# Optimization experiments

Hardware: AMD Instinct MI355X
Metric: run time of the kernel (lower is better)

The kernel has to match this reference:

```python
import jax, jax.numpy as jnp
import numpy as np

M = 10000; D = 10000; FG = 256; FD = 256; K = 64
EX = 320000; EY = 320000


def setup_inputs() -> dict:
    key = jax.random.key(0)
    ks = jax.random.split(key, 32)
    s = 0.05  # weight scale
    inp = {}
    inp['x_m'] = jax.random.normal(ks[0], (M, FG), jnp.float32)
    inp['x_d'] = jax.random.normal(ks[1], (D, FD), jnp.float32)
    inp['edge_index_x'] = jax.random.randint(ks[2], (2, EX), 0, M)
    inp['edge_index_y'] = jax.random.randint(ks[3], (2, EY), 0, D)
    # GAT layer params (PyG layout: W [in, H*C], att [H, C], bias [H*C])
    inp['Wx1'] = jax.random.normal(ks[4], (FG, 2 * FG), jnp.float32) * s
    inp['ax1_src'] = jax.random.normal(ks[5], (2, FG), jnp.float32) * s
    inp['ax1_dst'] = jax.random.normal(ks[6], (2, FG), jnp.float32) * s
    inp['bx1'] = jnp.zeros((2 * FG,), jnp.float32)
    inp['Wx2'] = jax.random.normal(ks[7], (2 * FG, FG), jnp.float32) * s
    inp['ax2_src'] = jax.random.normal(ks[8], (1, FG), jnp.float32) * s
    inp['ax2_dst'] = jax.random.normal(ks[9], (1, FG), jnp.float32) * s
    inp['bx2'] = jnp.zeros((FG,), jnp.float32)
    inp['Wy1'] = jax.random.normal(ks[10], (FD, 2 * FD), jnp.float32) * s
    inp['ay1_src'] = jax.random.normal(ks[11], (2, FD), jnp.float32) * s
    inp['ay1_dst'] = jax.random.normal(ks[12], (2, FD), jnp.float32) * s
    inp['by1'] = jnp.zeros((2 * FD,), jnp.float32)
    inp['Wy2'] = jax.random.normal(ks[13], (2 * FD, FD), jnp.float32) * s
    inp['ay2_src'] = jax.random.normal(ks[14], (1, FD), jnp.float32) * s
    inp['ay2_dst'] = jax.random.normal(ks[15], (1, FD), jnp.float32) * s
    inp['by2'] = jnp.zeros((FD,), jnp.float32)
    # MLP heads
    inp['lwx1'] = jax.random.normal(ks[16], (FG, 256), jnp.float32) * s
    inp['lbx1'] = jnp.zeros((256,), jnp.float32)
    inp['lwx2'] = jax.random.normal(ks[17], (256, 128), jnp.float32) * s
    inp['lbx2'] = jnp.zeros((128,), jnp.float32)
    inp['lwx3'] = jax.random.normal(ks[18], (128, K), jnp.float32) * s
    inp['lbx3'] = jnp.zeros((K,), jnp.float32)
    inp['lwy1'] = jax.random.normal(ks[19], (FD, 256), jnp.float32) * s
    inp['lby1'] = jnp.zeros((256,), jnp.float32)
    inp['lwy2'] = jax.random.normal(ks[20], (256, 128), jnp.float32) * s
    inp['lby2'] = jnp.zeros((128,), jnp.float32)
    inp['lwy3'] = jax.random.normal(ks[21], (128, K), jnp.float32) * s
    inp['lby3'] = jnp.zeros((K,), jnp.float32)
    return inp


def gat_conv(x, src, dst, W, a_src, a_dst, b, n):
    # PyG GATConv, add_self_loops=False, negative_slope=0.2, concat=True
    H, C = a_src.shape
    xp = (x @ W).reshape(-1, H, C)                      # [N, H, C]
    al_s = jnp.einsum('nhc,hc->nh', xp, a_src)          # [N, H]
    al_d = jnp.einsum('nhc,hc->nh', xp, a_dst)
    e = jax.nn.leaky_relu(al_s[src] + al_d[dst], 0.2)   # [E, H]
    # softmax over edges grouped by destination node
    mx = jax.ops.segment_max(e, dst, num_segments=n)
    ee = jnp.exp(e - mx[dst])
    denom = jax.ops.segment_sum(ee, dst, num_segments=n)
    alpha = ee / (denom[dst] + 1e-16)                   # [E, H]
    out = jax.ops.segment_sum(xp[src] * alpha[:, :, None], dst, num_segments=n)
    return out.reshape(n, H * C) + b


def mlp3(h, w1, b1, w2, b2, w3, b3):
    h = jax.nn.relu(h @ w1 + b1)
    h = jax.nn.relu(h @ w2 + b2)
    return jax.nn.relu(h @ w3 + b3)


def reference(x_m, x_d, edge_index_x, edge_index_y,
              Wx1, ax1_src, ax1_dst, bx1, Wx2, ax2_src, ax2_dst, bx2,
              Wy1, ay1_src, ay1_dst, by1, Wy2, ay2_src, ay2_dst, by2,
              lwx1, lbx1, lwx2, lbx2, lwx3, lbx3,
              lwy1, lby1, lwy2, lby2, lwy3, lby3):
    sx, dx = edge_index_x[0], edge_index_x[1]
    sy, dy = edge_index_y[0], edge_index_y[1]
    X1 = jax.nn.relu(gat_conv(x_m, sx, dx, Wx1, ax1_src, ax1_dst, bx1, M))
    X = jax.nn.relu(gat_conv(X1, sx, dx, Wx2, ax2_src, ax2_dst, bx2, M))
    Y1 = jax.nn.relu(gat_conv(x_d, sy, dy, Wy1, ay1_src, ay1_dst, by1, D))
    Y = jax.nn.relu(gat_conv(Y1, sy, dy, Wy2, ay2_src, ay2_dst, by2, D))
    x = mlp3(X, lwx1, lbx1, lwx2, lbx2, lwx3, lbx3)     # [M, K]
    y = mlp3(Y, lwy1, lby1, lwy2, lby2, lwy3, lby3)     # [D, K]
    return x @ y.T                                      # [M, D]
```

## Files before the change

kernel.cpp:

```cpp
#include <hip/hip_runtime.h>
#include <cstddef>

#define NODES 10000
#define EDGES 320000

typedef __attribute__((ext_vector_type(8))) short bf16x8;
typedef __attribute__((ext_vector_type(4))) float f32x4;

__device__ inline short bf16rn(float x){
    union { float f; unsigned u; } v; v.f = x;
    unsigned r = (v.u + 0x7FFFu + ((v.u >> 16) & 1u)) >> 16;
    return (short)r;
}
__device__ inline float bf16tof(short h){
    union { float f; unsigned u; } v; v.u = ((unsigned)(unsigned short)h) << 16;
    return v.f;
}

__global__ void count_kernel(const int* __restrict__ dst, int E, int* __restrict__ counts){
    int e = blockIdx.x*blockDim.x + threadIdx.x;
    if (e < E) atomicAdd(&counts[dst[e]], 1);
}

__global__ __launch_bounds__(1024) void scan_kernel(const int* __restrict__ counts,
                                                    int* __restrict__ rowptr, int N){
    __shared__ int part[1024];
    int t = threadIdx.x;
    int chunk = (N + 1023) / 1024;
    int b0 = t * chunk;
    int s = 0;
    for (int i=0;i<chunk;i++){ int idx=b0+i; if (idx<N) s += counts[idx]; }
    part[t] = s;
    __syncthreads();
    for (int off=1; off<1024; off<<=1){
        int v = (t>=off) ? part[t-off] : 0;
        __syncthreads();
        part[t] += v;
        __syncthreads();
    }
    int excl = (t==0) ? 0 : part[t-1];
    for (int i=0;i<chunk;i++){
        int idx=b0+i;
        if (idx<N){ rowptr[idx]=excl; excl += counts[idx]; }
    }
    if (t==1023) rowptr[N] = part[1023];
}

__global__ void fill_kernel(const int* __restrict__ src, const int* __restrict__ dst, int E,
                            int* __restrict__ cursor, int* __restrict__ col){
    int e = blockIdx.x*blockDim.x + threadIdx.x;
    if (e < E){
        int d = dst[e];
        int p = atomicAdd(&cursor[d], 1);
        col[p] = src[e];
    }
}

__global__ __launch_bounds__(256) void splitT(const float* __restrict__ B,
        short* __restrict__ Bth, short* __restrict__ Btl, int K, int N)
{
    __shared__ float tile[32][33];
    int tx = threadIdx.x, ty = threadIdx.y;
    int n0 = blockIdx.x * 32, k0 = blockIdx.y * 32;
    #pragma unroll
    for (int r=0;r<4;r++){
        int k = ty + r*8;
        tile[k][tx] = B[(size_t)(k0+k)*N + n0 + tx];
    }
    __syncthreads();
    #pragma unroll
    for (int r=0;r<4;r++){
        int n = ty + r*8;
        float v = tile[tx][n];
        short h = bf16rn(v);
        short l = bf16rn(v - bf16tof(h));
        Bth[(size_t)(n0+n)*K + k0 + tx] = h;
        Btl[(size_t)(n0+n)*K + k0 + tx] = l;
    }
}

__global__ void split_rows(const float* __restrict__ in, short* __restrict__ hi,
                           short* __restrict__ lo, int n)
{
    int i = (blockIdx.x*blockDim.x + threadIdx.x) * 4;
    if (i >= n) return;
    float4 v = *(const float4*)&in[i];
    short h0=bf16rn(v.x), h1=bf16rn(v.y), h2=bf16rn(v.z), h3=bf16rn(v.w);
    short4 hv; hv.x=h0; hv.y=h1; hv.z=h2; hv.w=h3;
    short4 lv; lv.x=bf16rn(v.x-bf16tof(h0)); lv.y=bf16rn(v.y-bf16tof(h1));
    lv.z=bf16rn(v.z-bf16tof(h2)); lv.w=bf16rn(v.w-bf16tof(h3));
    *(short4*)&hi[i] = hv;
    *(short4*)&lo[i] = lv;
}

__global__ __launch_bounds__(256) void gemm_split(
    const float* __restrict__ A,
    const short* __restrict__ Bh, const short* __restrict__ Bl,
    float* __restrict__ C, const float* __restrict__ bias,
    int Mr, int Nr, int Kr, int relu)
{
    constexpr int LD = 88;
    __shared__ short Ash[64][LD], Asl[64][LD], Bsh[64][LD], Bsl[64][LD];
    int t = threadIdx.x;
    int lane = t & 63, wave = t >> 6;
    int wm = (wave >> 1) * 32, wn = (wave & 1) * 32;
    int m0 = blockIdx.y * 64, n0 = blockIdx.x * 64;

    f32x4 acc[2][2];
    #pragma unroll
    for (int i=0;i<2;i++)
      #pragma unroll
      for (int j=0;j<2;j++)
        #pragma unroll
        for (int r=0;r<4;r++) acc[i][j][r] = 0.f;

    int ar = t >> 4;
    int ac = (t & 15) * 4;
    int br = t >> 3;
    int bc = (t & 7) * 8;

    for (int k0 = 0; k0 < Kr; k0 += 64){
        #pragma unroll
        for (int rep = 0; rep < 4; rep++){
            int row = ar + rep*16;
            float4 v = make_float4(0.f,0.f,0.f,0.f);
            if (m0 + row < Mr) v = *(const float4*)&A[(size_t)(m0+row)*Kr + k0 + ac];
            short h0=bf16rn(v.x), h1=bf16rn(v.y), h2=bf16rn(v.z), h3=bf16rn(v.w);
            short4 hv; hv.x=h0; hv.y=h1; hv.z=h2; hv.w=h3;
            short4 lv; lv.x=bf16rn(v.x-bf16tof(h0)); lv.y=bf16rn(v.y-bf16tof(h1));
            lv.z=bf16rn(v.z-bf16tof(h2)); lv.w=bf16rn(v.w-bf16tof(h3));
            *(short4*)&Ash[row][ac] = hv;
            *(short4*)&Asl[row][ac] = lv;
        }
        #pragma unroll
        for (int rep = 0; rep < 2; rep++){
            int row = br + rep*32;
            int gn = n0 + row;
            int4 hv = make_int4(0,0,0,0), lv = make_int4(0,0,0,0);
            if (gn < Nr){
                hv = *(const int4*)&Bh[(size_t)gn*Kr + k0 + bc];
                lv = *(const int4*)&Bl[(size_t)gn*Kr + k0 + bc];
            }
            *(int4*)&Bsh[row][bc] = hv;
            *(int4*)&Bsl[row][bc] = lv;
        }
        __syncthreads();
        #pragma unroll
        for (int ks = 0; ks < 2; ks++){
            int kk = ks*32 + (lane >> 4) * 8;
            bf16x8 ah[2], alo[2], bh[2], blo[2];
            #pragma unroll
            for (int i=0;i<2;i++){
                ah[i]  = *(const bf16x8*)&Ash[wm + i*16 + (lane&15)][kk];
                alo[i] = *(const bf16x8*)&Asl[wm + i*16 + (lane&15)][kk];
                bh[i]  = *(const bf16x8*)&Bsh[wn + i*16 + (lane&15)][kk];
                blo[i] = *(const bf16x8*)&Bsl[wn + i*16 + (lane&15)][kk];
            }
            #pragma unroll
            for (int i=0;i<2;i++)
              #pragma unroll
              for (int j=0;j<2;j++){
                  acc[i][j] = __builtin_amdgcn_mfma_f32_16x16x32_bf16(ah[i],  bh[j],  acc[i][j], 0,0,0);
                  acc[i][j] = __builtin_amdgcn_mfma_f32_16x16x32_bf16(alo[i], bh[j],  acc[i][j], 0,0,0);
                  acc[i][j] = __builtin_amdgcn_mfma_f32_16x16x32_bf16(ah[i],  blo[j], acc[i][j], 0,0,0);
              }
        }
        __syncthreads();
    }
    #pragma unroll
    for (int i=0;i<2;i++){
        int rbase = m0 + wm + i*16 + (lane>>4)*4;
        #pragma unroll
        for (int j=0;j<2;j++){
            int col = n0 + wn + j*16 + (lane&15);
            if (col >= Nr) continue;
            float bv = bias ? bias[col] : 0.f;
            #pragma unroll
            for (int r=0;r<4;r++){
                int row = rbase + r;
                if (row < Mr){
                    float v = acc[i][j][r] + bv;
                    if (relu) v = v > 0.f ? v : 0.f;
                    C[(size_t)row*Nr + col] = v;
                }
            }
        }
    }
}

__global__ __launch_bounds__(256) void al_kernel(const float* __restrict__ xp,
        const float* __restrict__ a_src, const float* __restrict__ a_dst,
        float* __restrict__ als, float* __restrict__ ald, int N, int H, int C)
{
    int n = blockIdx.x;
    int t = threadIdx.x;
    __shared__ float rs[4], rd[4];
    for (int h=0;h<H;h++){
        float ps=0.f, pd=0.f;
        for (int c=t;c<C;c+=256){
            float v = xp[(size_t)n*H*C + (size_t)h*C + c];
            ps += v * a_src[h*C+c];
            pd += v * a_dst[h*C+c];
        }
        #pragma unroll
        for (int off=32; off; off>>=1){
            ps += __shfl_down(ps, off);
            pd += __shfl_down(pd, off);
        }
        if ((t & 63) == 0){ rs[t>>6]=ps; rd[t>>6]=pd; }
        __syncthreads();
        if (t==0){
            als[n*H+h] = rs[0]+rs[1]+rs[2]+rs[3];
            ald[n*H+h] = rd[0]+rd[1]+rd[2]+rd[3];
        }
        __syncthreads();
    }
}

template<int H, int C>
__global__ __launch_bounds__(256) void gat_agg(const float* __restrict__ xp,
        const float* __restrict__ als, const float* __restrict__ ald,
        const int* __restrict__ rowptr, const int* __restrict__ col,
        const float* __restrict__ bias, float* __restrict__ out, int N)
{
    constexpr int W  = H*C;
    constexpr int PC = W/256;
    constexpr int CH = 128;
    int n = blockIdx.x;
    int t = threadIdx.x;
    int beg = rowptr[n], end = rowptr[n+1];
    int deg = end - beg;
    __shared__ float red[4];
    __shared__ float m_sh[H], den_sh[H];
    __shared__ int   sidx[CH];
    __shared__ float salpha[CH*H];

    float aldn[H];
    #pragma unroll
    for (int h=0;h<H;h++) aldn[h] = ald[n*H+h];

    for (int h=0;h<H;h++){
        float mx = -1e30f;
        for (int i=t;i<deg;i+=256){
            int s = col[beg+i];
            float e = als[s*H+h] + aldn[h];
            e = e>0.f ? e : 0.2f*e;
            mx = fmaxf(mx, e);
        }
        #pragma unroll
        for (int off=32; off; off>>=1) mx = fmaxf(mx, __shfl_down(mx,off));
        if ((t&63)==0) red[t>>6]=mx;
        __syncthreads();
        if (t==0) m_sh[h] = fmaxf(fmaxf(red[0],red[1]), fmaxf(red[2],red[3]));
        __syncthreads();
        float m = m_sh[h];
        float sm = 0.f;
        for (int i=t;i<deg;i+=256){
            int s = col[beg+i];
            float e = als[s*H+h] + aldn[h];
            e = e>0.f ? e : 0.2f*e;
            sm += expf(e - m);
        }
        #pragma unroll
        for (int off=32; off; off>>=1) sm += __shfl_down(sm,off);
        if ((t&63)==0) red[t>>6]=sm;
        __syncthreads();
        if (t==0) den_sh[h] = red[0]+red[1]+red[2]+red[3];
        __syncthreads();
    }

    float acc[PC];
    #pragma unroll
    for (int j=0;j<PC;j++) acc[j]=0.f;
    float invden[H], msh[H];
    #pragma unroll
    for (int h=0;h<H;h++){ invden[h] = 1.f/(den_sh[h]+1e-16f); msh[h]=m_sh[h]; }

    for (int c0=0;c0<deg;c0+=CH){
        int cl = min(CH, deg-c0);
        __syncthreads();
        if (t < cl){
            int s = col[beg+c0+t];
            sidx[t] = s;
            #pragma unroll
            for (int h=0;h<H;h++){
                float e = als[s*H+h] + aldn[h];
                e = e>0.f ? e : 0.2f*e;
                salpha[t*H+h] = expf(e - msh[h]) * invden[h];
            }
        }
        __syncthreads();
        for (int i=0;i<cl;i++){
            int s = sidx[i];
            const float* row = xp + (size_t)s*W;
            #pragma unroll
            for (int j=0;j<PC;j++){
                int cidx = t + j*256;
                acc[j] += salpha[i*H + (cidx/C)] * row[cidx];
            }
        }
    }
    #pragma unroll
    for (int j=0;j<PC;j++){
        int cidx = t + j*256;
        float v = acc[j] + bias[cidx];
        out[(size_t)n*W + cidx] = v>0.f ? v : 0.f;
    }
}

extern "C" void kernel_launch(void* const* d_in, const int* in_sizes, int n_in,
                              void* d_out, int out_size, void* d_ws, size_t ws_size,
                              hipStream_t stream)
{
    const float* x_m  = (const float*)d_in[0];
    const float* x_d  = (const float*)d_in[1];
    const int*   eix  = (const int*)d_in[2];
    const int*   eiy  = (const int*)d_in[3];
    const float* Wx1  = (const float*)d_in[4];
    const float* ax1s = (const float*)d_in[5];
    const float* ax1d = (const float*)d_in[6];
    const float* bx1  = (const float*)d_in[7];
    const float* Wx2  = (const float*)d_in[8];
    const float* ax2s = (const float*)d_in[9];
    const float* ax2d = (const float*)d_in[10];
    const float* bx2  = (const float*)d_in[11];
    const float* Wy1  = (const float*)d_in[12];
    const float* ay1s = (const float*)d_in[13];
    const float* ay1d = (const float*)d_in[14];
    const float* by1  = (const float*)d_in[15];
    const float* Wy2  = (const float*)d_in[16];
    const float* ay2s = (const float*)d_in[17];
    const float* ay2d = (const float*)d_in[18];
    const float* by2  = (const float*)d_in[19];
    const float* lwx1 = (const float*)d_in[20];
    const float* lbx1 = (const float*)d_in[21];
    const float* lwx2 = (const float*)d_in[22];
    const float* lbx2 = (const float*)d_in[23];
    const float* lwx3 = (const float*)d_in[24];
    const float* lbx3 = (const float*)d_in[25];
    const float* lwy1 = (const float*)d_in[26];
    const float* lby1 = (const float*)d_in[27];
    const float* lwy2 = (const float*)d_in[28];
    const float* lby2 = (const float*)d_in[29];
    const float* lwy3 = (const float*)d_in[30];
    const float* lby3 = (const float*)d_in[31];

    const int N = NODES, E = EDGES;
    char* ws = (char*)d_ws;
    size_t off = 0;
    auto alloc = [&](size_t bytes)->char*{
        size_t a = (off + 255) & ~(size_t)255;
        off = a + bytes;
        return ws + a;
    };
    int* rowptr   = (int*)alloc((size_t)(N+1)*sizeof(int));
    int* cursor   = (int*)alloc((size_t)N*sizeof(int));
    int* counts   = (int*)alloc((size_t)N*sizeof(int));
    int* colidx   = (int*)alloc((size_t)E*sizeof(int));
    float* xp     = (float*)alloc((size_t)N*512*sizeof(float));
    float* bufA   = (float*)alloc((size_t)N*512*sizeof(float));
    float* bufB   = (float*)alloc((size_t)N*256*sizeof(float));
    float* als    = (float*)alloc((size_t)N*2*sizeof(float));
    float* aldv   = (float*)alloc((size_t)N*2*sizeof(float));
    float* xf     = (float*)alloc((size_t)N*64*sizeof(float));
    float* yf     = (float*)alloc((size_t)N*64*sizeof(float));
    short* Bth    = (short*)alloc((size_t)512*512*sizeof(short));
    short* Btl    = (short*)alloc((size_t)512*512*sizeof(short));
    short* Yh     = (short*)alloc((size_t)N*64*sizeof(short));
    short* Yl     = (short*)alloc((size_t)N*64*sizeof(short));

    auto gemm = [&](const float* A, const float* W, float* C, const float* bias,
                    int Kr, int Nr, int relu)
    {
        splitT<<<dim3(Nr/32, Kr/32), dim3(32,8), 0, stream>>>(W, Bth, Btl, Kr, Nr);
        gemm_split<<<dim3((Nr+63)/64, (N+63)/64), 256, 0, stream>>>(
            A, Bth, Btl, C, bias, N, Nr, Kr, relu);
    };

    auto run_graph = [&](const float* xin, const int* ei,
                         const float* W1, const float* a1s, const float* a1d, const float* b1,
                         const float* W2, const float* a2s, const float* a2d, const float* b2,
                         const float* lw1, const float* lb1, const float* lw2, const float* lb2,
                         const float* lw3, const float* lb3, float* outv)
    {
        const int* srcp = ei;
        const int* dstp = ei + E;
        hipMemsetAsync(counts, 0, (size_t)N*sizeof(int), stream);
        count_kernel<<<(E+255)/256, 256, 0, stream>>>(dstp, E, counts);
        scan_kernel<<<1, 1024, 0, stream>>>(counts, rowptr, N);
        hipMemcpyAsync(cursor, rowptr, (size_t)N*sizeof(int), hipMemcpyDeviceToDevice, stream);
        fill_kernel<<<(E+255)/256, 256, 0, stream>>>(srcp, dstp, E, cursor, colidx);
        gemm(xin, W1, xp, nullptr, 256, 512, 0);
        al_kernel<<<N, 256, 0, stream>>>(xp, a1s, a1d, als, aldv, N, 2, 256);
        gat_agg<2,256><<<N, 256, 0, stream>>>(xp, als, aldv, rowptr, colidx, b1, bufA, N);
        gemm(bufA, W2, xp, nullptr, 512, 256, 0);
        al_kernel<<<N, 256, 0, stream>>>(xp, a2s, a2d, als, aldv, N, 1, 256);
        gat_agg<1,256><<<N, 256, 0, stream>>>(xp, als, aldv, rowptr, colidx, b2, bufB, N);
        gemm(bufB, lw1, bufA, lb1, 256, 256, 1);
        gemm(bufA, lw2, xp,   lb2, 256, 128, 1);
        gemm(xp,   lw3, outv, lb3, 128, 64,  1);
    };

    run_graph(x_m, eix, Wx1, ax1s, ax1d, bx1, Wx2, ax2s, ax2d, bx2,
              lwx1, lbx1, lwx2, lbx2, lwx3, lbx3, xf);
    run_graph(x_d, eiy, Wy1, ay1s, ay1d, by1, Wy2, ay2s, ay2d, by2,
              lwy1, lby1, lwy2, lby2, lwy3, lby3, yf);

    split_rows<<<(N*64/4 + 255)/256, 256, 0, stream>>>(yf, Yh, Yl, N*64);
    gemm_split<<<dim3((N+63)/64, (N+63)/64), 256, 0, stream>>>(
        xf, Yh, Yl, (float*)d_out, nullptr, N, N, 64, 0);
}
```

Measured before the change: 1.258 ms.

## Batch both graphs into shared kernels with presplit bf16 operands and precomputed attention

Processes the two graphs together: a combined CSR build, batched weight splitting, and two-job GEMM launches, so each stage runs as one launch instead of two. GEMM outputs are written directly as hi/lo bf16 pairs, which removes the per-tile fp32-to-bf16 split inside the GEMM. Attention logits come from a precomputed W·a vector (a GEMV on the layer input) instead of a pass over the projected features. Softmax coefficients are computed in a separate per-edge kernel before aggregation. The GEMM tile grows to 96 rows. The cost is more workspace memory and extra kernels for alpha and weight preprocessing.

Measured after the change: 1.148 ms. 1.1x faster.

```diff
diff --git a/kernel.cpp b/kernel.cpp
--- a/kernel.cpp
+++ b/kernel.cpp
@@ -1,5 +1,6 @@
 #include <hip/hip_runtime.h>
 #include <cstddef>
+#include <cstdint>
 
 #define NODES 10000
 #define EDGES 320000
@@ -17,9 +18,13 @@
     return v.f;
 }
 
-__global__ void count_kernel(const int* __restrict__ dst, int E, int* __restrict__ counts){
-    int e = blockIdx.x*blockDim.x + threadIdx.x;
-    if (e < E) atomicAdd(&counts[dst[e]], 1);
+__global__ void count2_kernel(const int* __restrict__ ex, const int* __restrict__ ey,
+                              int* __restrict__ counts){
+    int e = blockIdx.x*256 + threadIdx.x;
+    if (e < 2*EDGES){
+        int d = (e < EDGES) ? ex[EDGES + e] : (ey[e] + NODES);
+        atomicAdd(&counts[d], 1);
+    }
 }
 
 __global__ __launch_bounds__(1024) void scan_kernel(const int* __restrict__ counts,
@@ -46,265 +51,278 @@
     if (t==1023) rowptr[N] = part[1023];
 }
 
-__global__ void fill_kernel(const int* __restrict__ src, const int* __restrict__ dst, int E,
-                            int* __restrict__ cursor, int* __restrict__ col){
-    int e = blockIdx.x*blockDim.x + threadIdx.x;
-    if (e < E){
-        int d = dst[e];
+__global__ void fill2_kernel(const int* __restrict__ ex, const int* __restrict__ ey,
+                             int* __restrict__ cursor, int* __restrict__ col){
+    int e = blockIdx.x*256 + threadIdx.x;
+    if (e < 2*EDGES){
+        int s, d;
+        if (e < EDGES){ s = ex[e]; d = ex[EDGES+e]; }
+        else          { s = ey[e-EDGES] + NODES; d = ey[e] + NODES; }
         int p = atomicAdd(&cursor[d], 1);
-        col[p] = src[e];
-    }
-}
-
-__global__ __launch_bounds__(256) void splitT(const float* __restrict__ B,
-        short* __restrict__ Bth, short* __restrict__ Btl, int K, int N)
-{
+        col[p] = s;
+    }
+}
+
+struct WtJob { const float* W; const float* a; float* out; int K; int H; int h; };
+struct WtJobs { WtJob j[12]; };
+__global__ __launch_bounds__(256) void wtilde_kernel(WtJobs js){
+    WtJob jb = js.j[blockIdx.x];
+    const int C = 256;
+    for (int k = threadIdx.x; k < jb.K; k += 256){
+        const float* wr = jb.W + (size_t)k*(jb.H*C) + jb.h*C;
+        const float* ar = jb.a + jb.h*C;
+        float s = 0.f;
+        for (int c=0;c<C;c++) s += wr[c]*ar[c];
+        jb.out[k*jb.H + jb.h] = s;
+    }
+}
+
+struct StJob { const float* B; short* th; short* tl; int K; int N; };
+struct StJobs { StJob j[10]; };
+__global__ __launch_bounds__(256) void splitT_batch(StJobs js){
+    StJob jb = js.j[blockIdx.z];
+    int n0 = blockIdx.x*32, k0 = blockIdx.y*32;
+    if (n0 >= jb.N || k0 >= jb.K) return;
     __shared__ float tile[32][33];
     int tx = threadIdx.x, ty = threadIdx.y;
-    int n0 = blockIdx.x * 32, k0 = blockIdx.y * 32;
-    #pragma unroll
-    for (int r=0;r<4;r++){
-        int k = ty + r*8;
-        tile[k][tx] = B[(size_t)(k0+k)*N + n0 + tx];
-    }
+    #pragma unroll
+    for (int r=0;r<4;r++){ int k = ty + r*8; tile[k][tx] = jb.B[(size_t)(k0+k)*jb.N + n0 + tx]; }
     __syncthreads();
     #pragma unroll
     for (int r=0;r<4;r++){
         int n = ty + r*8;
         float v = tile[tx][n];
         short h = bf16rn(v);
-        short l = bf16rn(v - bf16tof(h));
-        Bth[(size_t)(n0+n)*K + k0 + tx] = h;
-        Btl[(size_t)(n0+n)*K + k0 + tx] = l;
-    }
-}
-
-__global__ void split_rows(const float* __restrict__ in, short* __restrict__ hi,
-                           short* __restrict__ lo, int n)
-{
-    int i = (blockIdx.x*blockDim.x + threadIdx.x) * 4;
-    if (i >= n) return;
-    float4 v = *(const float4*)&in[i];
+        jb.th[(size_t)(n0+n)*jb.K + k0 + tx] = h;
+        jb.tl[(size_t)(n0+n)*jb.K + k0 + tx] = bf16rn(v - bf16tof(h));
+    }
+}
+
+__global__ void split_in_kernel(const float* __restrict__ x0, const float* __restrict__ x1,
+                                short* __restrict__ h, short* __restrict__ l){
+    int i = (blockIdx.x*256 + threadIdx.x)*4;
+    const int HALF = NODES*256;
+    if (i >= 2*HALF) return;
+    const float* src = (i < HALF) ? (x0 + i) : (x1 + (i - HALF));
+    float4 v = *(const float4*)src;
     short h0=bf16rn(v.x), h1=bf16rn(v.y), h2=bf16rn(v.z), h3=bf16rn(v.w);
     short4 hv; hv.x=h0; hv.y=h1; hv.z=h2; hv.w=h3;
     short4 lv; lv.x=bf16rn(v.x-bf16tof(h0)); lv.y=bf16rn(v.y-bf16tof(h1));
     lv.z=bf16rn(v.z-bf16tof(h2)); lv.w=bf16rn(v.w-bf16tof(h3));
-    *(short4*)&hi[i] = hv;
-    *(short4*)&lo[i] = lv;
-}
-
-__global__ __launch_bounds__(256) void gemm_split(
-    const float* __restrict__ A,
-    const short* __restrict__ Bh, const short* __restrict__ Bl,
-    float* __restrict__ C, const float* __restrict__ bias,
-    int Mr, int Nr, int Kr, int relu)
+    *(short4*)&h[i] = hv;
+    *(short4*)&l[i] = lv;
+}
+
+struct GemmJob {
+    const short* Ah; const short* Al; const short* Bh; const short* Bl;
+    float* C; short* Ch; short* Cl; const float* bias;
+};
+__global__ __launch_bounds__(256) void gemm_ps(GemmJob j0, GemmJob j1,
+        int Mr, int Nr, int Kr, int relu)
 {
-    constexpr int LD = 88;
-    __shared__ short Ash[64][LD], Asl[64][LD], Bsh[64][LD], Bsl[64][LD];
+    GemmJob j = (blockIdx.z == 0) ? j0 : j1;
+    __shared__ short Ash[96][88], Asl[96][88], Bsh[64][88], Bsl[64][88];
     int t = threadIdx.x;
     int lane = t & 63, wave = t >> 6;
-    int wm = (wave >> 1) * 32, wn = (wave & 1) * 32;
-    int m0 = blockIdx.y * 64, n0 = blockIdx.x * 64;
-
-    f32x4 acc[2][2];
-    #pragma unroll
-    for (int i=0;i<2;i++)
+    int wm = (wave >> 1) * 48, wn = (wave & 1) * 32;
+    int m0 = blockIdx.y * 96, n0 = blockIdx.x * 64;
+
+    f32x4 acc[3][2];
+    #pragma unroll
+    for (int i=0;i<3;i++)
       #pragma unroll
-      for (int j=0;j<2;j++)
-        #pragma unroll
-        for (int r=0;r<4;r++) acc[i][j][r] = 0.f;
-
-    int ar = t >> 4;
-    int ac = (t & 15) * 4;
-    int br = t >> 3;
-    int bc = (t & 7) * 8;
+      for (int jj=0;jj<2;jj++)
+        #pragma unroll
+        for (int r=0;r<4;r++) acc[i][jj][r] = 0.f;
+
+    int arow = t >> 3;
+    int ablk = (t & 7) * 8;
 
     for (int k0 = 0; k0 < Kr; k0 += 64){
         #pragma unroll
-        for (int rep = 0; rep < 4; rep++){
-            int row = ar + rep*16;
-            float4 v = make_float4(0.f,0.f,0.f,0.f);
-            if (m0 + row < Mr) v = *(const float4*)&A[(size_t)(m0+row)*Kr + k0 + ac];
-            short h0=bf16rn(v.x), h1=bf16rn(v.y), h2=bf16rn(v.z), h3=bf16rn(v.w);
-            short4 hv; hv.x=h0; hv.y=h1; hv.z=h2; hv.w=h3;
-            short4 lv; lv.x=bf16rn(v.x-bf16tof(h0)); lv.y=bf16rn(v.y-bf16tof(h1));
-            lv.z=bf16rn(v.z-bf16tof(h2)); lv.w=bf16rn(v.w-bf16tof(h3));
-            *(short4*)&Ash[row][ac] = hv;
-            *(short4*)&Asl[row][ac] = lv;
-        }
-        #pragma unroll
-        for (int rep = 0; rep < 2; rep++){
-            int row = br + rep*32;
-            int gn = n0 + row;
-            int4 hv = make_int4(0,0,0,0), lv = make_int4(0,0,0,0);
-            if (gn < Nr){
-                hv = *(const int4*)&Bh[(size_t)gn*Kr + k0 + bc];
-                lv = *(const int4*)&Bl[(size_t)gn*Kr + k0 + bc];
-            }
-            *(int4*)&Bsh[row][bc] = hv;
-            *(int4*)&Bsl[row][bc] = lv;
+        for (int rep=0; rep<3; rep++){
+            int row = arow + rep*32;
+            int gr = m0 + row; gr = gr < Mr ? gr : Mr-1;
+            size_t off = (size_t)gr*Kr + k0 + ablk;
+            *(int4*)&Ash[row][ablk] = *(const int4*)&j.Ah[off];
+            *(int4*)&Asl[row][ablk] = *(const int4*)&j.Al[off];
+        }
+        #pragma unroll
+        for (int rep=0; rep<2; rep++){
+            int row = arow + rep*32;
+            int gn = n0 + row; gn = gn < Nr ? gn : Nr-1;
+            size_t off = (size_t)gn*Kr + k0 + ablk;
+            *(int4*)&Bsh[row][ablk] = *(const int4*)&j.Bh[off];
+            *(int4*)&Bsl[row][ablk] = *(const int4*)&j.Bl[off];
         }
         __syncthreads();
         #pragma unroll
-        for (int ks = 0; ks < 2; ks++){
-            int kk = ks*32 + (lane >> 4) * 8;
-            bf16x8 ah[2], alo[2], bh[2], blo[2];
+        for (int ks=0; ks<2; ks++){
+            int kk = ks*32 + (lane>>4)*8;
+            bf16x8 bh[2], bl[2];
             #pragma unroll
-            for (int i=0;i<2;i++){
-                ah[i]  = *(const bf16x8*)&Ash[wm + i*16 + (lane&15)][kk];
-                alo[i] = *(const bf16x8*)&Asl[wm + i*16 + (lane&15)][kk];
-                bh[i]  = *(const bf16x8*)&Bsh[wn + i*16 + (lane&15)][kk];
-                blo[i] = *(const bf16x8*)&Bsl[wn + i*16 + (lane&15)][kk];
+            for (int jj=0;jj<2;jj++){
+                bh[jj] = *(const bf16x8*)&Bsh[wn + jj*16 + (lane&15)][kk];
+                bl[jj] = *(const bf16x8*)&Bsl[wn + jj*16 + (lane&15)][kk];
             }
             #pragma unroll
-            for (int i=0;i<2;i++)
-              #pragma unroll
-              for (int j=0;j<2;j++){
-                  acc[i][j] = __builtin_amdgcn_mfma_f32_16x16x32_bf16(ah[i],  bh[j],  acc[i][j], 0,0,0);
-                  acc[i][j] = __builtin_amdgcn_mfma_f32_16x16x32_bf16(alo[i], bh[j],  acc[i][j], 0,0,0);
-                  acc[i][j] = __builtin_amdgcn_mfma_f32_16x16x32_bf16(ah[i],  blo[j], acc[i][j], 0,0,0);
-              }
+            for (int i=0;i<3;i++){
+                bf16x8 ah = *(const bf16x8*)&Ash[wm + i*16 + (lane&15)][kk];
+                bf16x8 al = *(const bf16x8*)&Asl[wm + i*16 + (lane&15)][kk];
+                #pragma unroll
+                for (int jj=0;jj<2;jj++){
+                    acc[i][jj] = __builtin_amdgcn_mfma_f32_16x16x32_bf16(ah, bh[jj], acc[i][jj], 0,0,0);
+                    acc[i][jj] = __builtin_amdgcn_mfma_f32_16x16x32_bf16(al, bh[jj], acc[i][jj], 0,0,0);
+                    acc[i][jj] = __builtin_amdgcn_mfma_f32_16x16x32_bf16(ah, bl[jj], acc[i][jj], 0,0,0);
+                }
+            }
         }
         __syncthreads();
     }
     #pragma unroll
-    for (int i=0;i<2;i++){
-        int rbase = m0 + wm + i*16 + (lane>>4)*4;
-        #pragma unroll
-        for (int j=0;j<2;j++){
-            int col = n0 + wn + j*16 + (lane&15);
-            if (col >= Nr) continue;
-            float bv = bias ? bias[col] : 0.f;
+    for (int i=0;i<3;i++){
+        int rbase = m0 + wm + i*16 + ((lane>>4)<<2);
+        #pragma unroll
+        for (int jj=0;jj<2;jj++){
+            int colg = n0 + wn + jj*16 + (lane&15);
+            if (colg >= Nr) continue;
+            float bv = j.bias ? j.bias[colg] : 0.f;
             #pragma unroll
             for (int r=0;r<4;r++){
-                int row = rbase + r;
-                if (row < Mr){
-                    float v = acc[i][j][r] + bv;
+                int rg = rbase + r;
+                if (rg < Mr){
+                    float v = acc[i][jj][r] + bv;
                     if (relu) v = v > 0.f ? v : 0.f;
-                    C[(size_t)row*Nr + col] = v;
+                    if (j.C) j.C[(size_t)rg*Nr + colg] = v;
+                    if (j.Ch){
+                        short hh = bf16rn(v);
+                        j.Ch[(size_t)rg*Nr + colg] = hh;
+                        j.Cl[(size_t)rg*Nr + colg] = bf16rn(v - bf16tof(hh));
+                    }
                 }
             }
         }
     }
 }
 
-__global__ __launch_bounds__(256) void al_kernel(const float* __restrict__ xp,
-        const float* __restrict__ a_src, const float* __restrict__ a_dst,
-        float* __restrict__ als, float* __restrict__ ald, int N, int H, int C)
+template<int H>
+__global__ __launch_bounds__(256) void algemv(const float* __restrict__ A0,
+        const float* __restrict__ A1, const float* __restrict__ wtS,
+        const float* __restrict__ wtD, int K,
+        float* __restrict__ als, float* __restrict__ ald)
 {
-    int n = blockIdx.x;
-    int t = threadIdx.x;
-    __shared__ float rs[4], rd[4];
-    for (int h=0;h<H;h++){
-        float ps=0.f, pd=0.f;
-        for (int c=t;c<C;c+=256){
-            float v = xp[(size_t)n*H*C + (size_t)h*C + c];
-            ps += v * a_src[h*C+c];
-            pd += v * a_dst[h*C+c];
-        }
-        #pragma unroll
-        for (int off=32; off; off>>=1){
-            ps += __shfl_down(ps, off);
-            pd += __shfl_down(pd, off);
-        }
-        if ((t & 63) == 0){ rs[t>>6]=ps; rd[t>>6]=pd; }
-        __syncthreads();
-        if (t==0){
-            als[n*H+h] = rs[0]+rs[1]+rs[2]+rs[3];
-            ald[n*H+h] = rd[0]+rd[1]+rd[2]+rd[3];
-        }
-        __syncthreads();
-    }
-}
-
-template<int H, int C>
-__global__ __launch_bounds__(256) void gat_agg(const float* __restrict__ xp,
-        const float* __restrict__ als, const float* __restrict__ ald,
-        const int* __restrict__ rowptr, const int* __restrict__ col,
-        const float* __restrict__ bias, float* __restrict__ out, int N)
+    int node = blockIdx.x*4 + (threadIdx.x>>6);
+    int lane = threadIdx.x & 63;
+    if (node >= 2*NODES) return;
+    int g = node >= NODES;
+    const float* A = g ? (A1 + (size_t)(node-NODES)*K) : (A0 + (size_t)node*K);
+    const float* ws = wtS + (size_t)g*K*H;
+    const float* wd = wtD + (size_t)g*K*H;
+    float ss[H], sd[H];
+    #pragma unroll
+    for (int h=0;h<H;h++){ ss[h]=0.f; sd[h]=0.f; }
+    for (int k=lane; k<K; k+=64){
+        float v = A[k];
+        #pragma unroll
+        for (int h=0;h<H;h++){ ss[h] += v*ws[k*H+h]; sd[h] += v*wd[k*H+h]; }
+    }
+    #pragma unroll
+    for (int off=32; off; off>>=1){
+        #pragma unroll
+        for (int h=0;h<H;h++){ ss[h] += __shfl_xor(ss[h], off); sd[h] += __shfl_xor(sd[h], off); }
+    }
+    if (lane==0){
+        #pragma unroll
+        for (int h=0;h<H;h++){ als[node*H+h]=ss[h]; ald[node*H+h]=sd[h]; }
+    }
+}
+
+template<int H>
+__global__ __launch_bounds__(256) void alpha_kernel(const int* __restrict__ rowptr,
+        const int* __restrict__ col, const float* __restrict__ als,
+        const float* __restrict__ ald, float* __restrict__ alpha)
 {
-    constexpr int W  = H*C;
-    constexpr int PC = W/256;
-    constexpr int CH = 128;
-    int n = blockIdx.x;
-    int t = threadIdx.x;
-    int beg = rowptr[n], end = rowptr[n+1];
-    int deg = end - beg;
-    __shared__ float red[4];
-    __shared__ float m_sh[H], den_sh[H];
-    __shared__ int   sidx[CH];
-    __shared__ float salpha[CH*H];
-
-    float aldn[H];
-    #pragma unroll
-    for (int h=0;h<H;h++) aldn[h] = ald[n*H+h];
-
-    for (int h=0;h<H;h++){
+    int node = blockIdx.x*4 + (threadIdx.x>>6);
+    int lane = threadIdx.x & 63;
+    if (node >= 2*NODES) return;
+    int beg = rowptr[node], end = rowptr[node+1];
+    #pragma unroll
+    for (int h=0; h<H; h++){
+        float ad = ald[node*H+h];
         float mx = -1e30f;
-        for (int i=t;i<deg;i+=256){
-            int s = col[beg+i];
-            float e = als[s*H+h] + aldn[h];
+        for (int p=beg+lane; p<end; p+=64){
+            float e = als[col[p]*H+h] + ad;
             e = e>0.f ? e : 0.2f*e;
             mx = fmaxf(mx, e);
         }
         #pragma unroll
-        for (int off=32; off; off>>=1) mx = fmaxf(mx, __shfl_down(mx,off));
-        if ((t&63)==0) red[t>>6]=mx;
-        __syncthreads();
-        if (t==0) m_sh[h] = fmaxf(fmaxf(red[0],red[1]), fmaxf(red[2],red[3]));
-        __syncthreads();
-        float m = m_sh[h];
+        for (int off=32; off; off>>=1) mx = fmaxf(mx, __shfl_xor(mx, off));
         float sm = 0.f;
-        for (int i=t;i<deg;i+=256){
-            int s = col[beg+i];
-            float e = als[s*H+h] + aldn[h];
+        for (int p=beg+lane; p<end; p+=64){
+            float e = als[col[p]*H+h] + ad;
             e = e>0.f ? e : 0.2f*e;
-            sm += expf(e - m);
-        }
-        #pragma unroll
-        for (int off=32; off; off>>=1) sm += __shfl_down(sm,off);
-        if ((t&63)==0) red[t>>6]=sm;
-        __syncthreads();
-        if (t==0) den_sh[h] = red[0]+red[1]+red[2]+red[3];
-        __syncthreads();
-    }
-
-    float acc[PC];
-    #pragma unroll
-    for (int j=0;j<PC;j++) acc[j]=0.f;
-    float invden[H], msh[H];
-    #pragma unroll
-    for (int h=0;h<H;h++){ invden[h] = 1.f/(den_sh[h]+1e-16f); msh[h]=m_sh[h]; }
-
-    for (int c0=0;c0<deg;c0+=CH){
-        int cl = min(CH, deg-c0);
-        __syncthreads();
-        if (t < cl){
-            int s = col[beg+c0+t];
-            sidx[t] = s;
-            #pragma unroll
-            for (int h=0;h<H;h++){
-                float e = als[s*H+h] + aldn[h];
-                e = e>0.f ? e : 0.2f*e;
-                salpha[t*H+h] = expf(e - msh[h]) * invden[h];
-            }
-        }
-        __syncthreads();
-        for (int i=0;i<cl;i++){
-            int s = sidx[i];
-            const float* row = xp + (size_t)s*W;
-            #pragma unroll
-            for (int j=0;j<PC;j++){
-                int cidx = t + j*256;
-                acc[j] += salpha[i*H + (cidx/C)] * row[cidx];
-            }
-        }
-    }
-    #pragma unroll
-    for (int j=0;j<PC;j++){
-        int cidx = t + j*256;
-        float v = acc[j] + bias[cidx];
-        out[(size_t)n*W + cidx] = v>0.f ? v : 0.f;
+            sm += __expf(e - mx);
+        }
+        #pragma unroll
+        for (int off=32; off; off>>=1) sm += __shfl_xor(sm, off);
+        float inv = 1.f/(sm + 1e-16f);
+        for (int p=beg+lane; p<end; p+=64){
+            float e = als[col[p]*H+h] + ad;
+            e = e>0.f ? e : 0.2f*e;
+            alpha[(size_t)p*H + h] = __expf(e - mx)*inv;
+        }
+    }
+}
+
+template<int W, int H>
+__global__ __launch_bounds__(256) void agg_ps(const float* __restrict__ xp,
+        const float* __restrict__ alpha, const int* __restrict__ rowptr,
+        const int* __restrict__ col, const float* __restrict__ bias0,
+        const float* __restrict__ bias1, float* __restrict__ out,
+        short* __restrict__ outH, short* __restrict__ outL)
+{
+    int node = blockIdx.x*4 + (threadIdx.x>>6);
+    int lane = threadIdx.x & 63;
+    if (node >= 2*NODES) return;
+    int beg = rowptr[node], end = rowptr[node+1];
+    constexpr int NF = W/64;
+    int lb = lane*NF;
+    int hsel = (H==2) ? (lane>>5) : 0;
+    float4 a0 = make_float4(0.f,0.f,0.f,0.f);
+    float4 a1 = make_float4(0.f,0.f,0.f,0.f);
+    for (int p=beg; p<end; p++){
+        int s = col[p];
+        float av = alpha[(size_t)p*H + hsel];
+        const float* row = xp + (size_t)s*W + lb;
+        float4 v0 = *(const float4*)row;
+        a0.x += av*v0.x; a0.y += av*v0.y; a0.z += av*v0.z; a0.w += av*v0.w;
+        if (NF==8){
+            float4 v1 = *(const float4*)(row+4);
+            a1.x += av*v1.x; a1.y += av*v1.y; a1.z += av*v1.z; a1.w += av*v1.w;
+        }
+    }
+    const float* bs = (node >= NODES) ? bias1 : bias0;
+    float4 bv = *(const float4*)&bs[lb];
+    float r0 = fmaxf(a0.x+bv.x, 0.f), r1 = fmaxf(a0.y+bv.y, 0.f);
+    float r2 = fmaxf(a0.z+bv.z, 0.f), r3 = fmaxf(a0.w+bv.w, 0.f);
+    size_t base = (size_t)node*W + lb;
+    if (out){ float4 o = make_float4(r0,r1,r2,r3); *(float4*)&out[base] = o; }
+    short4 hh, ll;
+    hh.x=bf16rn(r0); hh.y=bf16rn(r1); hh.z=bf16rn(r2); hh.w=bf16rn(r3);
+    ll.x=bf16rn(r0-bf16tof(hh.x)); ll.y=bf16rn(r1-bf16tof(hh.y));
+    ll.z=bf16rn(r2-bf16tof(hh.z)); ll.w=bf16rn(r3-bf16tof(hh.w));
+    *(short4*)&outH[base] = hh;
+    *(short4*)&outL[base] = ll;
+    if (NF==8){
+        float4 bw = *(const float4*)&bs[lb+4];
+        float s0 = fmaxf(a1.x+bw.x, 0.f), s1 = fmaxf(a1.y+bw.y, 0.f);
+        float s2 = fmaxf(a1.z+bw.z, 0.f), s3 = fmaxf(a1.w+bw.w, 0.f);
+        if (out){ float4 o = make_float4(s0,s1,s2,s3); *(float4*)&out[base+4] = o; }
+        hh.x=bf16rn(s0); hh.y=bf16rn(s1); hh.z=bf16rn(s2); hh.w=bf16rn(s3);
+        ll.x=bf16rn(s0-bf16tof(hh.x)); ll.y=bf16rn(s1-bf16tof(hh.y));
+        ll.z=bf16rn(s2-bf16tof(hh.z)); ll.w=bf16rn(s3-bf16tof(hh.w));
+        *(short4*)&outH[base+4] = hh;
+        *(short4*)&outL[base+4] = ll;
     }
 }
 
@@ -345,7 +363,7 @@
     const float* lwy3 = (const float*)d_in[30];
     const float* lby3 = (const float*)d_in[31];
 
-    const int N = NODES, E = EDGES;
+    const int N = NODES, E = EDGES, N2 = 2*NODES;
     char* ws = (char*)d_ws;
     size_t off = 0;
     auto alloc = [&](size_t bytes)->char*{
@@ -353,60 +371,120 @@
         off = a + bytes;
         return ws + a;
     };
-    int* rowptr   = (int*)alloc((size_t)(N+1)*sizeof(int));
-    int* cursor   = (int*)alloc((size_t)N*sizeof(int));
-    int* counts   = (int*)alloc((size_t)N*sizeof(int));
-    int* colidx   = (int*)alloc((size_t)E*sizeof(int));
-    float* xp     = (float*)alloc((size_t)N*512*sizeof(float));
-    float* bufA   = (float*)alloc((size_t)N*512*sizeof(float));
-    float* bufB   = (float*)alloc((size_t)N*256*sizeof(float));
-    float* als    = (float*)alloc((size_t)N*2*sizeof(float));
-    float* aldv   = (float*)alloc((size_t)N*2*sizeof(float));
-    float* xf     = (float*)alloc((size_t)N*64*sizeof(float));
-    float* yf     = (float*)alloc((size_t)N*64*sizeof(float));
-    short* Bth    = (short*)alloc((size_t)512*512*sizeof(short));
-    short* Btl    = (short*)alloc((size_t)512*512*sizeof(short));
-    short* Yh     = (short*)alloc((size_t)N*64*sizeof(short));
-    short* Yl     = (short*)alloc((size_t)N*64*sizeof(short));
-
-    auto gemm = [&](const float* A, const float* W, float* C, const float* bias,
-                    int Kr, int Nr, int relu)
-    {
-        splitT<<<dim3(Nr/32, Kr/32), dim3(32,8), 0, stream>>>(W, Bth, Btl, Kr, Nr);
-        gemm_split<<<dim3((Nr+63)/64, (N+63)/64), 256, 0, stream>>>(
-            A, Bth, Btl, C, bias, N, Nr, Kr, relu);
-    };
-
-    auto run_graph = [&](const float* xin, const int* ei,
-                         const float* W1, const float* a1s, const float* a1d, const float* b1,
-                         const float* W2, const float* a2s, const float* a2d, const float* b2,
-                         const float* lw1, const float* lb1, const float* lw2, const float* lb2,
-                         const float* lw3, const float* lb3, float* outv)
-    {
-        const int* srcp = ei;
-        const int* dstp = ei + E;
-        hipMemsetAsync(counts, 0, (size_t)N*sizeof(int), stream);
-        count_kernel<<<(E+255)/256, 256, 0, stream>>>(dstp, E, counts);
-        scan_kernel<<<1, 1024, 0, stream>>>(counts, rowptr, N);
-        hipMemcpyAsync(cursor, rowptr, (size_t)N*sizeof(int), hipMemcpyDeviceToDevice, stream);
-        fill_kernel<<<(E+255)/256, 256, 0, stream>>>(srcp, dstp, E, cursor, colidx);
-        gemm(xin, W1, xp, nullptr, 256, 512, 0);
-        al_kernel<<<N, 256, 0, stream>>>(xp, a1s, a1d, als, aldv, N, 2, 256);
-        gat_agg<2,256><<<N, 256, 0, stream>>>(xp, als, aldv, rowptr, colidx, b1, bufA, N);
-        gemm(bufA, W2, xp, nullptr, 512, 256, 0);
-        al_kernel<<<N, 256, 0, stream>>>(xp, a2s, a2d, als, aldv, N, 1, 256);
-        gat_agg<1,256><<<N, 256, 0, stream>>>(xp, als, aldv, rowptr, colidx, b2, bufB, N);
-        gemm(bufB, lw1, bufA, lb1, 256, 256, 1);
-        gemm(bufA, lw2, xp,   lb2, 256, 128, 1);
-        gemm(xp,   lw3, outv, lb3, 128, 64,  1);
-    };
-
-    run_graph(x_m, eix, Wx1, ax1s, ax1d, bx1, Wx2, ax2s, ax2d, bx2,
-              lwx1, lbx1, lwx2, lbx2, lwx3, lbx3, xf);
-    run_graph(x_d, eiy, Wy1, ay1s, ay1d, by1, Wy2, ay2s, ay2d, by2,
-              lwy1, lby1, lwy2, lby2, lwy3, lby3, yf);
-
-    split_rows<<<(N*64/4 + 255)/256, 256, 0, stream>>>(yf, Yh, Yl, N*64);
-    gemm_split<<<dim3((N+63)/64, (N+63)/64), 256, 0, stream>>>(
-        xf, Yh, Yl, (float*)d_out, nullptr, N, N, 64, 0);
-}
+    int* rowptr = (int*)alloc((size_t)(N2+1)*4);
+    int* cursor = (int*)alloc((size_t)N2*4);
+    int* counts = (int*)alloc((size_t)N2*4);
+    int* colidx = (int*)alloc((size_t)2*E*4);
+    float* alphaA = (float*)alloc((size_t)2*E*2*4);
+    short* xinh = (short*)alloc((size_t)N2*256*2);
+    short* xinl = (short*)alloc((size_t)N2*256*2);
+    float* xp   = (float*)alloc((size_t)N2*512*4);
+    float* als1 = (float*)alloc((size_t)N2*2*4);
+    float* ald1 = (float*)alloc((size_t)N2*2*4);
+    float* bufA = (float*)alloc((size_t)N2*512*4);
+    short* bufAh = (short*)alloc((size_t)N2*512*2);
+    short* bufAl = (short*)alloc((size_t)N2*512*2);
+    float* xp2  = (float*)alloc((size_t)N2*256*4);
+    float* als2 = (float*)alloc((size_t)N2*4);
+    float* ald2 = (float*)alloc((size_t)N2*4);
+    short* bufBh = (short*)alloc((size_t)N2*256*2);
+    short* bufBl = (short*)alloc((size_t)N2*256*2);
+    short* m1h = (short*)alloc((size_t)N2*256*2);
+    short* m1l = (short*)alloc((size_t)N2*256*2);
+    short* m2h = (short*)alloc((size_t)N2*128*2);
+    short* m2l = (short*)alloc((size_t)N2*128*2);
+    short* m3h = (short*)alloc((size_t)N2*64*2);
+    short* m3l = (short*)alloc((size_t)N2*64*2);
+    float* wt1s = (float*)alloc((size_t)2*256*2*4);
+    float* wt1d = (float*)alloc((size_t)2*256*2*4);
+    float* wt2s = (float*)alloc((size_t)2*512*4);
+    float* wt2d = (float*)alloc((size_t)2*512*4);
+    auto sal = [&](size_t n)->short*{ return (short*)alloc(n*2); };
+    short* w1h0 = sal(512*256), *w1l0 = sal(512*256), *w1h1 = sal(512*256), *w1l1 = sal(512*256);
+    short* w2h0 = sal(256*512), *w2l0 = sal(256*512), *w2h1 = sal(256*512), *w2l1 = sal(256*512);
+    short* l1h0 = sal(256*256), *l1l0 = sal(256*256), *l1h1 = sal(256*256), *l1l1 = sal(256*256);
+    short* l2h0 = sal(128*256), *l2l0 = sal(128*256), *l2h1 = sal(128*256), *l2l1 = sal(128*256);
+    short* l3h0 = sal(64*128),  *l3l0 = sal(64*128),  *l3h1 = sal(64*128),  *l3l1 = sal(64*128);
+
+    hipMemsetAsync(counts, 0, (size_t)N2*4, stream);
+    count2_kernel<<<(2*E+255)/256, 256, 0, stream>>>(eix, eiy, counts);
+    scan_kernel<<<1, 1024, 0, stream>>>(counts, rowptr, N2);
+    hipMemcpyAsync(cursor, rowptr, (size_t)N2*4, hipMemcpyDeviceToDevice, stream);
+    fill2_kernel<<<(2*E+255)/256, 256, 0, stream>>>(eix, eiy, cursor, colidx);
+
+    WtJobs wj;
+    wj.j[0] = {Wx1, ax1s, wt1s,         256, 2, 0};
+    wj.j[1] = {Wx1, ax1s, wt1s,         256, 2, 1};
+    wj.j[2] = {Wx1, ax1d, wt1d,         256, 2, 0};
+    wj.j[3] = {Wx1, ax1d, wt1d,         256, 2, 1};
+    wj.j[4] = {Wy1, ay1s, wt1s+256*2,   256, 2, 0};
+    wj.j[5] = {Wy1, ay1s, wt1s+256*2,   256, 2, 1};
+    wj.j[6] = {Wy1, ay1d, wt1d+256*2,   256, 2, 0};
+    wj.j[7] = {Wy1, ay1d, wt1d+256*2,   256, 2, 1};
+    wj.j[8] = {Wx2, ax2s, wt2s,         512, 1, 0};
+    wj.j[9] = {Wx2, ax2d, wt2d,         512, 1, 0};
+    wj.j[10]= {Wy2, ay2s, wt2s+512,     512, 1, 0};
+    wj.j[11]= {Wy2, ay2d, wt2d+512,     512, 1, 0};
+    wtilde_kernel<<<12, 256, 0, stream>>>(wj);
+
+    StJobs sj;
+    sj.j[0] = {Wx1,  w1h0, w1l0, 256, 512};
+    sj.j[1] = {Wy1,  w1h1, w1l1, 256, 512};
+    sj.j[2] = {Wx2,  w2h0, w2l0, 512, 256};
+    sj.j[3] = {Wy2,  w2h1, w2l1, 512, 256};
+    sj.j[4] = {lwx1, l1h0, l1l0, 256, 256};
+    sj.j[5] = {lwy1, l1h1, l1l1, 256, 256};
+    sj.j[6] = {lwx2, l2h0, l2l0, 256, 128};
+    sj.j[7] = {lwy2, l2h1, l2l1, 256, 128};
+    sj.j[8] = {lwx3, l3h0, l3l0, 128, 64};
+    sj.j[9] = {lwy3, l3h1, l3l1, 128, 64};
+    splitT_batch<<<dim3(16,16,10), dim3(32,8), 0, stream>>>(sj);
+
+    split_in_kernel<<<(N2*256/4 + 255)/256, 256, 0, stream>>>(x_m, x_d, xinh, xinl);
+
+    GemmJob jz = {nullptr,nullptr,nullptr,nullptr,nullptr,nullptr,nullptr,nullptr};
+
+    {
+        GemmJob a = {xinh, xinl, w1h0, w1l0, xp, nullptr, nullptr, nullptr};
+        GemmJob b = {xinh + (size_t)N*256, xinl + (size_t)N*256, w1h1, w1l1,
+                     xp + (size_t)N*512, nullptr, nullptr, nullptr};
+        gemm_ps<<<dim3(8, (N+95)/96, 2), 256, 0, stream>>>(a, b, N, 512, 256, 0);
+    }
+    algemv<2><<<(N2+3)/4, 256, 0, stream>>>(x_m, x_d, wt1s, wt1d, 256, als1, ald1);
+    alpha_kernel<2><<<(N2+3)/4, 256, 0, stream>>>(rowptr, colidx, als1, ald1, alphaA);
+    agg_ps<512,2><<<(N2+3)/4, 256, 0, stream>>>(xp, alphaA, rowptr, colidx,
+                                                bx1, by1, bufA, bufAh, bufAl);
+    {
+        GemmJob a = {bufAh, bufAl, w2h0, w2l0, xp2, nullptr, nullptr, nullptr};
+        GemmJob b = {bufAh + (size_t)N*512, bufAl + (size_t)N*512, w2h1, w2l1,
+                     xp2 + (size_t)N*256, nullptr, nullptr, nullptr};
+        gemm_ps<<<dim3(4, (N+95)/96, 2), 256, 0, stream>>>(a, b, N, 256, 512, 0);
+    }
+    algemv<1><<<(N2+3)/4, 256, 0, stream>>>(bufA, bufA + (size_t)N*512, wt2s, wt2d, 512, als2, ald2);
+    alpha_kernel<1><<<(N2+3)/4, 256, 0, stream>>>(rowptr, colidx, als2, ald2, alphaA);
+    agg_ps<256,1><<<(N2+3)/4, 256, 0, stream>>>(xp2, alphaA, rowptr, colidx,
+                                                bx2, by2, nullptr, bufBh, bufBl);
+    {
+        GemmJob a = {bufBh, bufBl, l1h0, l1l0, nullptr, m1h, m1l, lbx1};
+        GemmJob b = {bufBh + (size_t)N*256, bufBl + (size_t)N*256, l1h1, l1l1,
+                     nullptr, m1h + (size_t)N*256, m1l + (size_t)N*256, lby1};
+        gemm_ps<<<dim3(4, (N+95)/96, 2), 256, 0, stream>>>(a, b, N, 256, 256, 1);
+    }
+    {
+        GemmJob a = {m1h, m1l, l2h0, l2l0, nullptr, m2h, m2l, lbx2};
+        GemmJob b = {m1h + (size_t)N*256, m1l + (size_t)N*256, l2h1, l2l1,
+                     nullptr, m2h + (size_t)N*128, m2l + (size_t)N*128, lby2};
+        gemm_ps<<<dim3(2, (N+95)/96, 2), 256, 0, stream>>>(a, b, N, 128, 256, 1);
+    }
+    {
+        GemmJob a = {m2h, m2l, l3h0, l3l0, nullptr, m3h, m3l, lbx3};
+        GemmJob b = {m2h + (size_t)N*128, m2l + (size_t)N*128, l3h1, l3l1,
+                     nullptr, m3h + (size_t)N*64, m3l + (size_t)N*64, lby3};
+        gemm_ps<<<dim3(1, (N+95)/96, 2), 256, 0, stream>>>(a, b, N, 64, 128, 1);
+    }
+    {
+        GemmJob a = {m3h, m3l, m3h + (size_t)N*64, m3l + (size_t)N*64,
+                     (float*)d_out, nullptr, nullptr, nullptr};
+        gemm_ps<<<dim3((N+63)/64, (N+95)/96, 1), 256, 0, stream>>>(a, jz, N, N, 64, 0);
+    }
+}
```
